# Performance work log

Hardware: AMD Instinct MI355X
Metric: run time of the kernel (lower is better)

The kernel has to match this reference:

```python
import jax, jax.numpy as jnp
import numpy as np
from jax import lax

IOU_THRESHOLD = 0.5
TOP = 1000


def setup_inputs() -> dict:
    key = jax.random.key(0)
    k1, k2, k3, k4, k5 = jax.random.split(key, 5)
    B, P = 16, 20000
    # valid (x1, y1, x2, y2) boxes on an ~800x800 image
    x1 = jax.random.uniform(k1, (B, P)) * 800.0
    y1 = jax.random.uniform(k2, (B, P)) * 800.0
    w = jax.random.uniform(k3, (B, P)) * 200.0 + 1.0
    h = jax.random.uniform(k4, (B, P)) * 200.0 + 1.0
    reg = jnp.stack([x1, y1, x1 + w, y1 + h], axis=-1)  # [B, P, 4]
    cls = jax.random.normal(k5, (B, P))                  # [B, P]
    return {"reg": reg, "cls": cls}


def _pairwise_iou(boxes):
    """boxes: [B, N, 4] (x1,y1,x2,y2) -> IoU [B, N, N]."""
    a = boxes[:, :, None, :]  # [B, N, 1, 4]
    b = boxes[:, None, :, :]  # [B, 1, N, 4]
    xx1 = jnp.maximum(a[..., 0], b[..., 0])
    yy1 = jnp.maximum(a[..., 1], b[..., 1])
    xx2 = jnp.minimum(a[..., 2], b[..., 2])
    yy2 = jnp.minimum(a[..., 3], b[..., 3])
    inter = jnp.clip(xx2 - xx1, 0.0) * jnp.clip(yy2 - yy1, 0.0)
    area_a = (a[..., 2] - a[..., 0]) * (a[..., 3] - a[..., 1])
    area_b = (b[..., 2] - b[..., 0]) * (b[..., 3] - b[..., 1])
    return inter / (area_a + area_b - inter)


def reference(reg, cls):
    B = cls.shape[0]
    # sort by confidence descending, gather boxes, keep top
    order = jnp.argsort(-cls, axis=1)                      # [B, P]
    sorted_cls = jnp.take_along_axis(cls, order, axis=1)[:, :TOP]            # [B, N]
    sorted_reg = jnp.take_along_axis(reg, order[:, :, None], axis=1)[:, :TOP]  # [B, N, 4]
    N = sorted_cls.shape[1]

    iou = _pairwise_iou(sorted_reg)                        # [B, N, N]

    # sequential greedy suppression: if box i still kept, drop boxes with IoU>=thr
    def body(mask, i):
        keep_i = mask[:, i]                                # [B]
        tmp = iou[:, i, :] < IOU_THRESHOLD                 # [B, N]
        upd = (mask & tmp).at[:, i].set(True)
        new_mask = jnp.where(keep_i[:, None], upd, mask)
        return new_mask, None

    mask0 = jnp.ones((B, N), dtype=bool)
    mask, _ = lax.scan(body, mask0, jnp.arange(N))

    out_reg = jnp.where(mask[:, :, None], sorted_reg, 0.0)
    out_cls = jnp.where(mask, sorted_cls, 0.0)
    return out_reg, out_cls
```

## Files before the change

### kernel.cpp

```cpp
#include <hip/hip_runtime.h>
#include <stdint.h>

#define BATCH 16
#define NPTS  20000
#define TOPK  1000
#define NKPT  20
#define NBIN  2048
#define NCOPY 4
#define CANDCAP 2048

__device__ __forceinline__ uint32_t key_desc(float f) {
    uint32_t u = __float_as_uint(f);
    uint32_t m = (u & 0x80000000u) ? ~u : (u | 0x80000000u);
    return ~m;
}

__device__ __forceinline__ float key_undo(uint32_t k) {
    uint32_t m = ~k;
    uint32_t u = (m & 0x80000000u) ? (m & 0x7FFFFFFFu) : ~m;
    return __uint_as_float(u);
}

__device__ __forceinline__ void hist_scan_find(
    uint32_t (*wh)[NBIN], uint32_t* wsum, uint32_t* wpre,
    int* sh_T, int* sh_r, int* sh_binc,
    int tid, int wave, int lane, uint32_t r)
{
    uint32_t m0 = 0, m1 = 0;
    #pragma unroll
    for (int cpy = 0; cpy < NCOPY; ++cpy) { m0 += wh[cpy][2*tid]; m1 += wh[cpy][2*tid+1]; }
    uint32_t s = m0 + m1, x = s;
    #pragma unroll
    for (int d = 1; d < 64; d <<= 1) { uint32_t t = __shfl_up(x, d); if (lane >= d) x += t; }
    if (lane == 63) wsum[wave] = x;
    __syncthreads();
    if (wave == 0 && lane < 16) {
        uint32_t v = wsum[lane], y = v;
        #pragma unroll
        for (int d = 1; d < 16; d <<= 1) { uint32_t t = __shfl_up(y, d); if (lane >= d) y += t; }
        wpre[lane] = y - v;
    }
    __syncthreads();
    uint32_t e = wpre[wave] + (x - s);
    if (r >= e && r < e + s) {
        if (r < e + m0) { *sh_T = 2*tid;     *sh_r = (int)(r - e);      *sh_binc = (int)m0; }
        else            { *sh_T = 2*tid + 1; *sh_r = (int)(r - e - m0); *sh_binc = (int)m1; }
    }
}

__device__ __forceinline__ void push64(bool pred, uint64_t val, int* cntr,
                                       uint64_t* list, int lane) {
    uint64_t mask = __ballot(pred);
    if (mask) {
        int first = __ffsll((long long)mask) - 1;
        int base = 0;
        if (lane == first) base = atomicAdd(cntr, (int)__popcll(mask));
        base = __shfl(base, first);
        if (pred) {
            int off = (int)__popcll(mask & ((1ull << lane) - 1ull));
            list[base + off] = val;
        }
    }
}

__device__ __forceinline__ void wave_select(const uint64_t* lst, int n, int r,
                                            uint64_t* out, int wave, int lane) {
    if (wave == 0) {
        uint64_t my = (lane < n) ? lst[lane] : ~0ull;
        int rank = 0;
        for (int i = 0; i < n; ++i) { uint64_t o = __shfl(my, i); if (o < my) rank++; }
        if (lane < n && rank == r) *out = my;
    }
}

__device__ uint64_t bit_search(const uint32_t* klds, uint64_t known, uint64_t kmask,
                               int startbit, uint32_t r, int* sh_c,
                               int tid, int lane) {
    for (int bit = startbit; bit >= 0; --bit) {
        if (tid == 0) *sh_c = 0;
        __syncthreads();
        uint32_t local = 0;
        #pragma unroll
        for (int j = 0; j < NKPT; ++j) {
            int p = tid + j * 1024;
            if (p < NPTS) {
                uint64_t k64 = ((uint64_t)klds[p] << 32) | (uint32_t)p;
                if ((k64 & kmask) == known && !((k64 >> bit) & 1ull)) local++;
            }
        }
        #pragma unroll
        for (int d = 1; d < 64; d <<= 1) local += __shfl_xor(local, d);
        if (lane == 0 && local) atomicAdd(sh_c, (int)local);
        __syncthreads();
        uint32_t c0 = (uint32_t)*sh_c;
        if (r >= c0) { known |= 1ull << bit; r -= c0; }
        kmask |= 1ull << bit;
        __syncthreads();
    }
    return known;
}

__global__ __launch_bounds__(1024) void topk_kernel(
    const float* __restrict__ reg, const float* __restrict__ cls,
    float4* __restrict__ ws_boxes, float* __restrict__ ws_cls)
{
    __shared__ uint32_t klds[NPTS];
    __shared__ uint32_t whist[NCOPY][NBIN];
    __shared__ uint32_t wsum[16], wpre[16];
    __shared__ int      sh_T, sh_r, sh_binc, sh_cnt;
    __shared__ uint64_t sh_kthkey;
    __shared__ uint64_t cand[CANDCAP];
    __shared__ uint64_t cand2[64];
    __shared__ uint64_t sel[1024];

    const int b = blockIdx.x, tid = threadIdx.x;
    const int wave = tid >> 6, lane = tid & 63;
    const float* c = cls + (size_t)b * NPTS;

    #pragma unroll
    for (int i = 0; i < NCOPY * NBIN / 1024; ++i) ((uint32_t*)whist)[tid + i * 1024] = 0;
    #pragma unroll
    for (int j = 0; j < NKPT; ++j) {
        int p = tid + j * 1024;
        if (p < NPTS) klds[p] = key_desc(c[p]);
    }
    __syncthreads();

    #pragma unroll
    for (int j = 0; j < NKPT; ++j) {
        int p = tid + j * 1024;
        if (p < NPTS) atomicAdd(&whist[wave >> 2][klds[p] >> 21], 1u);
    }
    __syncthreads();
    hist_scan_find(whist, wsum, wpre, &sh_T, &sh_r, &sh_binc, tid, wave, lane, TOPK - 1);
    __syncthreads();
    const int T1 = sh_T; int r = sh_r; const int cnt1 = sh_binc;
    uint64_t known = (uint64_t)(uint32_t)T1 << 53;

    if (cnt1 <= 64) {
        if (tid == 0) sh_cnt = 0;
        __syncthreads();
        #pragma unroll
        for (int j = 0; j < NKPT; ++j) {
            int p = tid + j * 1024;
            uint32_t k = (p < NPTS) ? klds[p] : 0xFFFFFFFFu;
            push64(p < NPTS && (k >> 21) == (uint32_t)T1,
                   ((uint64_t)k << 32) | (uint32_t)p, &sh_cnt, cand2, lane);
        }
        __syncthreads();
        wave_select(cand2, cnt1, r, &sh_kthkey, wave, lane);
        __syncthreads();
    } else if (cnt1 <= CANDCAP) {
        if (tid == 0) sh_cnt = 0;
        __syncthreads();
        #pragma unroll
        for (int j = 0; j < NKPT; ++j) {
            int p = tid + j * 1024;
            uint32_t k = (p < NPTS) ? klds[p] : 0xFFFFFFFFu;
            push64(p < NPTS && (k >> 21) == (uint32_t)T1,
                   ((uint64_t)k << 32) | (uint32_t)p, &sh_cnt, cand, lane);
        }
        __syncthreads();
        #pragma unroll
        for (int i = 0; i < NCOPY * NBIN / 1024; ++i) ((uint32_t*)whist)[tid + i * 1024] = 0;
        __syncthreads();
        for (int i = tid; i < cnt1; i += 1024)
            atomicAdd(&whist[wave >> 2][(uint32_t)((cand[i] >> 42) & 2047)], 1u);
        __syncthreads();
        hist_scan_find(whist, wsum, wpre, &sh_T, &sh_r, &sh_binc, tid, wave, lane, (uint32_t)r);
        __syncthreads();
        const int T2 = sh_T; r = sh_r; const int cnt2 = sh_binc;
        known |= (uint64_t)(uint32_t)T2 << 42;
        if (cnt2 <= 64) {
            if (tid == 0) sh_cnt = 0;
            __syncthreads();
            for (int i = tid; i < cnt1; i += 1024)
                push64(((cand[i] >> 42) & 2047) == (uint64_t)(uint32_t)T2,
                       cand[i], &sh_cnt, cand2, lane);
            __syncthreads();
            wave_select(cand2, cnt2, r, &sh_kthkey, wave, lane);
            __syncthreads();
        } else {
            uint64_t kk = bit_search(klds, known, 0xFFFFFC0000000000ull, 41,
                                     (uint32_t)r, &sh_cnt, tid, lane);
            if (tid == 0) sh_kthkey = kk;
            __syncthreads();
        }
    } else {
        uint64_t kk = bit_search(klds, known, 0xFFE0000000000000ull, 52,
                                 (uint32_t)r, &sh_cnt, tid, lane);
        if (tid == 0) sh_kthkey = kk;
        __syncthreads();
    }
    const uint64_t kthkey = sh_kthkey;

    if (tid == 0) sh_cnt = 0;
    sel[tid] = ~0ull;
    __syncthreads();
    #pragma unroll
    for (int j = 0; j < NKPT; ++j) {
        int p = tid + j * 1024;
        uint64_t key = (p < NPTS) ? (((uint64_t)klds[p] << 32) | (uint32_t)p) : ~0ull;
        push64(key <= kthkey, key, &sh_cnt, sel, lane);
    }
    __syncthreads();

    uint64_t v = sel[tid];
    for (int k = 2; k <= 1024; k <<= 1) {
        for (int j = k >> 1; j >= 64; j >>= 1) {
            __syncthreads();
            sel[tid] = v;
            __syncthreads();
            uint64_t o = sel[tid ^ j];
            bool upper = (tid & j) != 0;
            bool asc   = (tid & k) == 0;
            v = (upper == asc) ? (v > o ? v : o) : (v < o ? v : o);
        }
        int j0 = (k >> 1) < 64 ? (k >> 1) : 32;
        for (int j = j0; j >= 1; j >>= 1) {
            uint64_t o = __shfl_xor(v, j);
            bool upper = (tid & j) != 0;
            bool asc   = (tid & k) == 0;
            v = (upper == asc) ? (v > o ? v : o) : (v < o ? v : o);
        }
    }

    if (tid < TOPK) {
        int p = (int)(v & 0xFFFFFFFFull);
        ws_boxes[b * TOPK + tid] = ((const float4*)reg)[(size_t)b * NPTS + p];
        ws_cls[b * TOPK + tid] = key_undo((uint32_t)(v >> 32));
    }
}

__global__ __launch_bounds__(256) void iou_kernel(
    const float4* __restrict__ ws_boxes, uint32_t* __restrict__ suppT)
{
    __shared__ float4 boxes[TOPK];
    __shared__ float  areas[TOPK];
    const int b     = blockIdx.y;
    const int chunk = blockIdx.x;
    const int tid   = threadIdx.x;
    for (int j = tid; j < TOPK; j += 256) {
        float4 v = ws_boxes[b * TOPK + j];
        boxes[j] = v;
        areas[j] = (v.z - v.x) * (v.w - v.y);
    }
    __syncthreads();

    const int lane = tid & 63;
    const int wave = tid >> 6;
    const int rbeg = chunk * 63;
    const int rend = (rbeg + 63 < TOPK) ? (rbeg + 63) : TOPK;
    uint32_t* t = suppT + (size_t)b * 32 * 1024;

    for (int i = rbeg + wave; i < rend; i += 4) {
        float4 a = boxes[i];
        float areaA = areas[i];
        uint64_t mine = 0;
        #pragma unroll
        for (int w = 0; w < 16; ++w) {
            int col = (w << 6) | lane;
            bool sup = false;
            if (col < TOPK) {
                float4 bb = boxes[col];
                float xx1 = fmaxf(a.x, bb.x);
                float yy1 = fmaxf(a.y, bb.y);
                float xx2 = fminf(a.z, bb.z);
                float yy2 = fminf(a.w, bb.w);
                float iw = fmaxf(xx2 - xx1, 0.0f);
                float ih = fmaxf(yy2 - yy1, 0.0f);
                float inter = iw * ih;
                float areaB = areas[col];
                float iou = inter / (areaA + areaB - inter);
                sup = (iou >= 0.5f);
            }
            uint64_t m = __ballot(sup);
            if (lane == w) mine = m;
        }
        if (lane < 16) {
            t[(2 * lane + 0) * 1024 + i] = (uint32_t)(mine & 0xFFFFFFFFull);
            t[(2 * lane + 1) * 1024 + i] = (uint32_t)(mine >> 32);
        }
    }
}

__global__ __launch_bounds__(64) void sweep_kernel(
    const uint32_t* __restrict__ suppT, const float4* __restrict__ ws_boxes,
    const float* __restrict__ ws_cls, float* __restrict__ out)
{
    const int b    = blockIdx.x;
    const int lane = threadIdx.x;
    const int myw  = lane & 31;
    const uint32_t* base = suppT + (size_t)b * 32 * 1024;

    uint32_t remv = 0, keptw = 0;
    uint4 dgA[8], clA[8], dgB[8], clB[8];

#define LOADG(W, DG, CL) { \
    const uint4* dp_ = (const uint4*)(base + (W) * 1024 + (W) * 32); \
    const uint4* cp_ = (const uint4*)(base + myw * 1024 + (W) * 32); \
    _Pragma("unroll") \
    for (int k_ = 0; k_ < 8; ++k_) { DG[k_] = dp_[k_]; CL[k_] = cp_[k_]; } }

#define STEP(D, C, BBIT) { \
    uint32_t live_ = (((~cur) >> (BBIT)) & 1u) & (uint32_t)((BBIT) < nb); \
    uint32_t msk_ = (uint32_t)0 - live_; \
    kmask |= (live_ << (BBIT)); \
    cur  |= (D) & msk_; \
    acc  |= (C) & msk_; }

#define PROC(W, DG, CL) { \
    const int nb = ((W) == 31) ? (TOPK - 31 * 32) : 32; \
    uint32_t cur = __shfl(remv, (W)); \
    uint32_t kmask = 0, acc = 0; \
    _Pragma("unroll") \
    for (int k_ = 0; k_ < 8; ++k_) { \
        STEP(DG[k_].x, CL[k_].x, 4 * k_ + 0); \
        STEP(DG[k_].y, CL[k_].y, 4 * k_ + 1); \
        STEP(DG[k_].z, CL[k_].z, 4 * k_ + 2); \
        STEP(DG[k_].w, CL[k_].w, 4 * k_ + 3); \
    } \
    remv |= acc; \
    if (myw == (W)) keptw = kmask; }

    LOADG(0, dgA, clA);
    #pragma unroll 1
    for (int w2 = 0; w2 < 16; ++w2) {
        const int wE = 2 * w2, wO = 2 * w2 + 1;
        LOADG(wO, dgB, clB);
        PROC(wE, dgA, clA);
        if (wO + 1 < 32) LOADG(wO + 1, dgA, clA);
        PROC(wO, dgB, clB);
    }

    __shared__ uint32_t skept[32];
    if (lane < 32) skept[lane] = keptw;
    __syncthreads();

    const float4* bx = ws_boxes + (size_t)b * TOPK;
    const float*  bc = ws_cls + (size_t)b * TOPK;
    float4* outr = (float4*)out + (size_t)b * TOPK;
    float*  outc = out + (size_t)BATCH * TOPK * 4 + (size_t)b * TOPK;
    for (int j = lane; j < TOPK; j += 64) {
        uint32_t keep = (skept[j >> 5] >> (j & 31)) & 1u;
        float4 v = bx[j];
        float cv = bc[j];
        outr[j] = keep ? v : make_float4(0.f, 0.f, 0.f, 0.f);
        outc[j] = keep ? cv : 0.0f;
    }
#undef LOADG
#undef STEP
#undef PROC
}

extern "C" void kernel_launch(void* const* d_in, const int* in_sizes, int n_in,
                              void* d_out, int out_size, void* d_ws, size_t ws_size,
                              hipStream_t stream) {
    (void)in_sizes; (void)n_in; (void)out_size; (void)ws_size;
    const float* reg = (const float*)d_in[0];
    const float* cls = (const float*)d_in[1];
    float* out = (float*)d_out;
    char* ws = (char*)d_ws;

    float4*   ws_boxes = (float4*)ws;
    float*    ws_cls   = (float*)(ws + 256000);
    uint32_t* suppT    = (uint32_t*)(ws + 320000);

    topk_kernel<<<dim3(BATCH), dim3(1024), 0, stream>>>(reg, cls, ws_boxes, ws_cls);
    iou_kernel<<<dim3(16, BATCH), dim3(256), 0, stream>>>(ws_boxes, suppT);
    sweep_kernel<<<dim3(BATCH), dim3(64), 0, stream>>>(suppT, ws_boxes, ws_cls, out);
}
```

Before: 74.24 us.

## Fuse IoU and sweep via last-block counter, rank-sort top-k, skip lower IoU triangle

Merges the IoU-mask kernel and the greedy sweep into one launch. Each batch's blocks bump an atomic counter, and the last block to finish runs the sweep and writes the output. The top-k kernel's bitonic sort is replaced by a rank count: each element counts the smaller entries in shared memory and scatters itself to that position. The IoU loop also skips 64-column words that lie entirely below the diagonal, since the sweep never reads them. The aim is to cut one kernel launch, the sort's barrier-heavy stages and about half the IoU arithmetic. The cost is a 1024-read linear scan per thread and added atomic and threadfence overhead.

```diff
diff --git a/kernel.cpp b/kernel.cpp
--- a/kernel.cpp
+++ b/kernel.cpp
@@ -102,7 +102,8 @@
 
 __global__ __launch_bounds__(1024) void topk_kernel(
     const float* __restrict__ reg, const float* __restrict__ cls,
-    float4* __restrict__ ws_boxes, float* __restrict__ ws_cls)
+    float4* __restrict__ ws_boxes, float* __restrict__ ws_cls,
+    uint32_t* __restrict__ done)
 {
     __shared__ uint32_t klds[NPTS];
     __shared__ uint32_t whist[NCOPY][NBIN];
@@ -116,6 +117,8 @@
     const int b = blockIdx.x, tid = threadIdx.x;
     const int wave = tid >> 6, lane = tid & 63;
     const float* c = cls + (size_t)b * NPTS;
+
+    if (tid == 0) done[b] = 0;
 
     #pragma unroll
     for (int i = 0; i < NCOPY * NBIN / 1024; ++i) ((uint32_t*)whist)[tid + i * 1024] = 0;
@@ -205,38 +208,27 @@
     }
     __syncthreads();
 
-    uint64_t v = sel[tid];
-    for (int k = 2; k <= 1024; k <<= 1) {
-        for (int j = k >> 1; j >= 64; j >>= 1) {
-            __syncthreads();
-            sel[tid] = v;
-            __syncthreads();
-            uint64_t o = sel[tid ^ j];
-            bool upper = (tid & j) != 0;
-            bool asc   = (tid & k) == 0;
-            v = (upper == asc) ? (v > o ? v : o) : (v < o ? v : o);
-        }
-        int j0 = (k >> 1) < 64 ? (k >> 1) : 32;
-        for (int j = j0; j >= 1; j >>= 1) {
-            uint64_t o = __shfl_xor(v, j);
-            bool upper = (tid & j) != 0;
-            bool asc   = (tid & k) == 0;
-            v = (upper == asc) ? (v > o ? v : o) : (v < o ? v : o);
-        }
-    }
-
-    if (tid < TOPK) {
-        int p = (int)(v & 0xFFFFFFFFull);
-        ws_boxes[b * TOPK + tid] = ((const float4*)reg)[(size_t)b * NPTS + p];
-        ws_cls[b * TOPK + tid] = key_undo((uint32_t)(v >> 32));
-    }
-}
-
-__global__ __launch_bounds__(256) void iou_kernel(
-    const float4* __restrict__ ws_boxes, uint32_t* __restrict__ suppT)
+    uint64_t e = sel[tid];
+    int rk = 0;
+    #pragma unroll 4
+    for (int m2 = 0; m2 < 1024; ++m2) rk += (sel[m2] < e) ? 1 : 0;
+    if (e != ~0ull) {
+        int p = (int)(e & 0xFFFFFFFFull);
+        ws_boxes[b * TOPK + rk] = ((const float4*)reg)[(size_t)b * NPTS + p];
+        ws_cls[b * TOPK + rk] = key_undo((uint32_t)(e >> 32));
+    }
+}
+
+__global__ __launch_bounds__(256) void iou_sweep_kernel(
+    const float4* __restrict__ ws_boxes, const float* __restrict__ ws_cls,
+    uint32_t* __restrict__ suppT, uint32_t* __restrict__ done,
+    float* __restrict__ out)
 {
     __shared__ float4 boxes[TOPK];
     __shared__ float  areas[TOPK];
+    __shared__ int    sh_last;
+    __shared__ uint32_t skept[32];
+
     const int b     = blockIdx.y;
     const int chunk = blockIdx.x;
     const int tid   = threadIdx.x;
@@ -257,8 +249,7 @@
         float4 a = boxes[i];
         float areaA = areas[i];
         uint64_t mine = 0;
-        #pragma unroll
-        for (int w = 0; w < 16; ++w) {
+        for (int w = i >> 6; w < 16; ++w) {
             int col = (w << 6) | lane;
             bool sup = false;
             if (col < TOPK) {
@@ -270,8 +261,7 @@
                 float iw = fmaxf(xx2 - xx1, 0.0f);
                 float ih = fmaxf(yy2 - yy1, 0.0f);
                 float inter = iw * ih;
-                float areaB = areas[col];
-                float iou = inter / (areaA + areaB - inter);
+                float iou = inter / (areaA + areas[col] - inter);
                 sup = (iou >= 0.5f);
             }
             uint64_t m = __ballot(sup);
@@ -282,19 +272,20 @@
             t[(2 * lane + 1) * 1024 + i] = (uint32_t)(mine >> 32);
         }
     }
-}
-
-__global__ __launch_bounds__(64) void sweep_kernel(
-    const uint32_t* __restrict__ suppT, const float4* __restrict__ ws_boxes,
-    const float* __restrict__ ws_cls, float* __restrict__ out)
-{
-    const int b    = blockIdx.x;
-    const int lane = threadIdx.x;
-    const int myw  = lane & 31;
+
+    __threadfence();
+    __syncthreads();
+    if (tid == 0) sh_last = (atomicAdd(&done[b], 1u) == 15u) ? 1 : 0;
+    __syncthreads();
+    if (!sh_last) return;
+    __threadfence();
+
     const uint32_t* base = suppT + (size_t)b * 32 * 1024;
-
-    uint32_t remv = 0, keptw = 0;
-    uint4 dgA[8], clA[8], dgB[8], clB[8];
+    uint32_t keptw = 0;
+    if (tid < 64) {
+        const int myw = tid & 31;
+        uint32_t remv = 0;
+        uint4 dgA[8], clA[8], dgB[8], clB[8];
 
 #define LOADG(W, DG, CL) { \
     const uint4* dp_ = (const uint4*)(base + (W) * 1024 + (W) * 32); \
@@ -323,34 +314,33 @@
     remv |= acc; \
     if (myw == (W)) keptw = kmask; }
 
-    LOADG(0, dgA, clA);
-    #pragma unroll 1
-    for (int w2 = 0; w2 < 16; ++w2) {
-        const int wE = 2 * w2, wO = 2 * w2 + 1;
-        LOADG(wO, dgB, clB);
-        PROC(wE, dgA, clA);
-        if (wO + 1 < 32) LOADG(wO + 1, dgA, clA);
-        PROC(wO, dgB, clB);
-    }
-
-    __shared__ uint32_t skept[32];
-    if (lane < 32) skept[lane] = keptw;
+        LOADG(0, dgA, clA);
+        #pragma unroll 1
+        for (int w2 = 0; w2 < 16; ++w2) {
+            const int wE = 2 * w2, wO = 2 * w2 + 1;
+            LOADG(wO, dgB, clB);
+            PROC(wE, dgA, clA);
+            if (wO + 1 < 32) LOADG(wO + 1, dgA, clA);
+            PROC(wO, dgB, clB);
+        }
+#undef LOADG
+#undef STEP
+#undef PROC
+    }
+    if (tid < 32) skept[tid] = keptw;
     __syncthreads();
 
     const float4* bx = ws_boxes + (size_t)b * TOPK;
     const float*  bc = ws_cls + (size_t)b * TOPK;
     float4* outr = (float4*)out + (size_t)b * TOPK;
     float*  outc = out + (size_t)BATCH * TOPK * 4 + (size_t)b * TOPK;
-    for (int j = lane; j < TOPK; j += 64) {
+    for (int j = tid; j < TOPK; j += 256) {
         uint32_t keep = (skept[j >> 5] >> (j & 31)) & 1u;
         float4 v = bx[j];
         float cv = bc[j];
         outr[j] = keep ? v : make_float4(0.f, 0.f, 0.f, 0.f);
         outc[j] = keep ? cv : 0.0f;
     }
-#undef LOADG
-#undef STEP
-#undef PROC
 }
 
 extern "C" void kernel_launch(void* const* d_in, const int* in_sizes, int n_in,
@@ -365,8 +355,8 @@
     float4*   ws_boxes = (float4*)ws;
     float*    ws_cls   = (float*)(ws + 256000);
     uint32_t* suppT    = (uint32_t*)(ws + 320000);
-
-    topk_kernel<<<dim3(BATCH), dim3(1024), 0, stream>>>(reg, cls, ws_boxes, ws_cls);
-    iou_kernel<<<dim3(16, BATCH), dim3(256), 0, stream>>>(ws_boxes, suppT);
-    sweep_kernel<<<dim3(BATCH), dim3(64), 0, stream>>>(suppT, ws_boxes, ws_cls, out);
-}
+    uint32_t* done     = (uint32_t*)(ws + 2417152);
+
+    topk_kernel<<<dim3(BATCH), dim3(1024), 0, stream>>>(reg, cls, ws_boxes, ws_cls, done);
+    iou_sweep_kernel<<<dim3(16, BATCH), dim3(256), 0, stream>>>(ws_boxes, ws_cls, suppT, done, out);
+}
```

New measurement: 138.9 us. 87.1% more time.
